# Performance work log

Measured on AMD Instinct MI355X. Metric: run time of the kernel, lower is better.

## Reference

```python
import jax, jax.numpy as jnp
import numpy as np

ALPHA = 0.2  # LeakyReLU negative slope
NEG_INF = -9e15


def setup_inputs() -> dict:
    key = jax.random.key(0)
    k1, k2, k3, k4, k5 = jax.random.split(key, 5)
    B, N, D = 4, 4096, 256
    feat = jax.random.normal(k1, (B, N, D), dtype=jnp.float32)
    adj = jax.random.randint(k2, (B, N, N), 0, 2, dtype=jnp.int32)
    W = jax.random.normal(k3, (D, D), dtype=jnp.float32) * (1.414 / np.sqrt(D))
    a_1 = jax.random.normal(k4, (D, 1), dtype=jnp.float32) * 0.1
    a_2 = jax.random.normal(k5, (D, 1), dtype=jnp.float32) * 0.1
    return {"feat": feat, "adj": adj, "W": W, "a_1": a_1, "a_2": a_2}


def reference(feat, adj, W, a_1, a_2):
    # h: [B, N, D]
    h = jnp.matmul(feat, W)
    Ax = jnp.matmul(h, a_1)  # [B, N, 1]
    Ay = jnp.matmul(h, a_2)  # [B, N, 1]
    # logits[b, i, j] = Ax[b, j] + Ay[b, i]
    logits = jnp.swapaxes(Ax, 1, 2) + Ay  # [B, N, N]
    e = jax.nn.leaky_relu(logits, negative_slope=ALPHA)
    e = jnp.where(adj > 0, e, jnp.float32(NEG_INF))
    attention = jax.nn.softmax(e, axis=-1)  # dropout p=0.0 -> identity
    h_prime = jnp.matmul(attention, feat)  # [B, N, in_features]
    h_out = jnp.matmul(h_prime, W)  # [B, N, out_features]
    return jax.nn.elu(h_out)
```

## Files before the change

kernel.cpp:

```cpp
#include <hip/hip_runtime.h>

typedef __attribute__((ext_vector_type(8))) short short8;
typedef __attribute__((ext_vector_type(4))) float f32x4;
typedef __attribute__((ext_vector_type(4))) int i32x4;
typedef __attribute__((ext_vector_type(2))) unsigned u32x2;

#define LOG2E 1.44269504f

__device__ __forceinline__ short f2bf(float f) {
  unsigned u = __builtin_bit_cast(unsigned, f);
  u += 0x7fffu + ((u >> 16) & 1u);
  return (short)(u >> 16);
}

__global__ void gat_wvec(const float* __restrict__ W, const float* __restrict__ a1,
                         const float* __restrict__ a2, float* __restrict__ w1,
                         float* __restrict__ w2) {
  __shared__ float a1f[256], a2f[256];
  const int tid = threadIdx.x;
  a1f[tid] = a1[tid];
  a2f[tid] = a2[tid];
  __syncthreads();
  float s1 = 0.f, s2 = 0.f;
  const float4* wr = (const float4*)(W + (size_t)tid * 256);
  for (int d0 = 0; d0 < 64; ++d0) {
    float4 v = wr[d0];
    s1 += v.x * a1f[d0 * 4] + v.y * a1f[d0 * 4 + 1] + v.z * a1f[d0 * 4 + 2] + v.w * a1f[d0 * 4 + 3];
    s2 += v.x * a2f[d0 * 4] + v.y * a2f[d0 * 4 + 1] + v.z * a2f[d0 * 4 + 2] + v.w * a2f[d0 * 4 + 3];
  }
  w1[tid] = s1;
  w2[tid] = s2;
}

__global__ void packB(const float* __restrict__ src, short* __restrict__ dst, int F) {
  const int tid = threadIdx.x;
  const int f = blockIdx.x, b = blockIdx.y;
  const int g = tid >> 4, l15 = tid & 15;
  const float* s = src + ((size_t)b * F * 32 + f * 32) * 256 + g * 16 + l15;
  short* d = dst + (((size_t)(b * F + f) * 16 + g) * 64) * 8;
#pragma unroll
  for (int q = 0; q < 4; ++q) {
    short8 v;
#pragma unroll
    for (int j8 = 0; j8 < 8; ++j8) v[j8] = f2bf(s[(q * 8 + j8) * 256]);
    *(short8*)(d + (q * 16 + l15) * 8) = v;
  }
}

__global__ void gat_axay(const float* __restrict__ feat, const float* __restrict__ w1,
                         const float* __restrict__ w2, float* __restrict__ AxL,
                         float* __restrict__ AyL) {
  const int lane = threadIdx.x & 63;
  const int row = blockIdx.x * 4 + (threadIdx.x >> 6);
  float4 fv = *(const float4*)(feat + (size_t)row * 256 + lane * 4);
  const float4 w1v = *(const float4*)(w1 + lane * 4);
  const float4 w2v = *(const float4*)(w2 + lane * 4);
  float s1 = fv.x * w1v.x + fv.y * w1v.y + fv.z * w1v.z + fv.w * w1v.w;
  float s2 = fv.x * w2v.x + fv.y * w2v.y + fv.z * w2v.z + fv.w * w2v.w;
#pragma unroll
  for (int off = 32; off >= 1; off >>= 1) {
    s1 += __shfl_xor(s1, off);
    s2 += __shfl_xor(s2, off);
  }
  if (lane == 0) { AxL[row] = s1 * LOG2E; AyL[row] = s2 * LOG2E; }
}

__global__ void gat_max(const float* __restrict__ AxL, float* __restrict__ MbL) {
  __shared__ float red[256];
  const int b = blockIdx.x, tid = threadIdx.x;
  float m = -3.4e38f;
  for (int i = tid; i < 4096; i += 256) m = fmaxf(m, AxL[b * 4096 + i]);
  red[tid] = m;
  __syncthreads();
  for (int s = 128; s > 0; s >>= 1) {
    if (tid < s) red[tid] = fmaxf(red[tid], red[tid + s]);
    __syncthreads();
  }
  if (tid == 0) MbL[b] = red[0];
}

__global__ __launch_bounds__(512, 4) void gat_attn(
    const short* __restrict__ featB,
    const int* __restrict__ adj,
    const float* __restrict__ AxL, const float* __restrict__ AyL,
    const float* __restrict__ MbL,
    const short* __restrict__ WB,
    float* __restrict__ out)
{
  __shared__ short smem[8448];

  const int tid = threadIdx.x;
  const int blk = blockIdx.x;
  const int x = blk & 7;
  const int b = x >> 1;
  const int it = ((blk >> 3) << 1) | (x & 1);
  const int i0 = it << 5;

  const int pi = tid >> 4;
  const int pj = tid & 15;
  const float ayL = AyL[b * 4096 + i0 + pi];
  const float sL = ayL + MbL[b];
  const float mrL = fmaxf(sL, 0.2f * sL);
  const float aL = ayL - mrL;
  const float dd = -0.8f * mrL;

  const int lane = tid & 63;
  const int w = tid >> 6;
  const int rowg = (w & 1) << 4;
  const int cgrp = (w >> 1) << 2;
  const int l15 = lane & 15;
  const int q = lane >> 4;

  f32x4 acc[4], lac;
  lac = (f32x4){0.f, 0.f, 0.f, 0.f};
#pragma unroll
  for (int j = 0; j < 4; ++j) acc[j] = (f32x4){0.f, 0.f, 0.f, 0.f};

  short8 ones;
#pragma unroll
  for (int j = 0; j < 8; ++j) ones[j] = (short)0x3F80;

  const i32x4* adjp = (const i32x4*)(adj + ((size_t)(b * 4096 + i0 + pi)) * 4096) + pj;
  const float4* axp = (const float4*)(AxL + b * 4096) + pj;
  const short* fbb = featB + (size_t)b * 128 * 16 * 64 * 8 + lane * 8;

  i32x4 adv = __builtin_nontemporal_load(adjp);
  float4 axv = axp[0];

  for (int jc = 0; jc < 64; ++jc) {
    const int pb = (jc & 1) * 2304;
    {
      const float* af = (const float*)&axv;
      unsigned pr[4];
#pragma unroll
      for (int u = 0; u < 4; ++u) {
        float v = af[u] + aL;
        float uu = fmaxf(v, fmaf(0.2f, v, dd));
        unsigned ub = adv[u] > 0 ? __builtin_bit_cast(unsigned, uu) : 0xFF800000u;
        float p = __builtin_amdgcn_exp2f(__builtin_bit_cast(float, ub));
        pr[u] = __builtin_bit_cast(unsigned, p) + 0x8000u;
      }
      u32x2 pw;
      pw[0] = __builtin_amdgcn_perm(pr[1], pr[0], 0x07060302u);
      pw[1] = __builtin_amdgcn_perm(pr[3], pr[2], 0x07060302u);
      *(u32x2*)(smem + pb + pi * 72 + pj * 4) = pw;
    }
    __syncthreads();

    if (jc < 63) {
      adv = __builtin_nontemporal_load(adjp + (jc + 1) * 16);
      axv = axp[(jc + 1) * 16];
    }

#pragma unroll
    for (int h = 0; h < 2; ++h) {
      const short* fb = fbb + (((size_t)(jc * 2 + h) * 16 + cgrp) << 9);
      short8 a = *(const short8*)(smem + pb + (rowg + l15) * 72 + h * 32 + q * 8);
      lac = __builtin_amdgcn_mfma_f32_16x16x32_bf16(a, ones, lac, 0, 0, 0);
#pragma unroll
      for (int ct = 0; ct < 4; ++ct) {
        short8 bf = *(const short8*)(fb + (ct << 9));
        acc[ct] = __builtin_amdgcn_mfma_f32_16x16x32_bf16(a, bf, acc[ct], 0, 0, 0);
      }
    }
  }

  float linv[4];
#pragma unroll
  for (int reg = 0; reg < 4; ++reg) {
    float l = lac[reg];
    linv[reg] = l > 0.f ? 1.f / l : 0.f;
  }

  __syncthreads();
  short* hbuf = smem;
#pragma unroll
  for (int reg = 0; reg < 4; ++reg) {
    const int lr = rowg + q * 4 + reg;
#pragma unroll
    for (int ct = 0; ct < 4; ++ct)
      hbuf[lr * 264 + cgrp * 16 + ct * 16 + l15] = f2bf(acc[ct][reg] * linv[reg]);
  }
  __syncthreads();

  f32x4 ac2[4];
#pragma unroll
  for (int j = 0; j < 4; ++j) ac2[j] = (f32x4){0.f, 0.f, 0.f, 0.f};

  const short* wbb = WB + lane * 8;
#pragma unroll
  for (int f = 0; f < 8; ++f) {
    short8 a = *(const short8*)&hbuf[(rowg + l15) * 264 + f * 32 + q * 8];
    const short* wb = wbb + (((size_t)f * 16 + cgrp) << 9);
#pragma unroll
    for (int ct = 0; ct < 4; ++ct) {
      short8 bf = *(const short8*)(wb + (ct << 9));
      ac2[ct] = __builtin_amdgcn_mfma_f32_16x16x32_bf16(a, bf, ac2[ct], 0, 0, 0);
    }
  }

#pragma unroll
  for (int reg = 0; reg < 4; ++reg) {
    const int row = i0 + rowg + q * 4 + reg;
    float* orow = out + ((size_t)(b * 4096 + row)) * 256 + cgrp * 16 + l15;
#pragma unroll
    for (int ct = 0; ct < 4; ++ct) {
      float v = ac2[ct][reg];
      float o = v > 0.f ? v : (__builtin_amdgcn_exp2f(v * LOG2E) - 1.f);
      __builtin_nontemporal_store(o, orow + ct * 16);
    }
  }
}

extern "C" void kernel_launch(void* const* d_in, const int* in_sizes, int n_in,
                              void* d_out, int out_size, void* d_ws, size_t ws_size,
                              hipStream_t stream) {
  (void)in_sizes; (void)n_in; (void)out_size; (void)ws_size;
  const float* feat = (const float*)d_in[0];
  const int* adj = (const int*)d_in[1];
  const float* W = (const float*)d_in[2];
  const float* a1 = (const float*)d_in[3];
  const float* a2 = (const float*)d_in[4];
  float* out = (float*)d_out;

  char* ws = (char*)d_ws;
  short* featB   = (short*)ws;
  short* WB      = (short*)(ws + 8388608);
  float* AxL     = (float*)(ws + 8519680);
  float* AyL     = (float*)(ws + 8585216);
  float* MbL     = (float*)(ws + 8650752);
  float* w1      = (float*)(ws + 8651776);
  float* w2      = (float*)(ws + 8652800);

  hipLaunchKernelGGL(gat_wvec, dim3(1), dim3(256), 0, stream, W, a1, a2, w1, w2);
  hipLaunchKernelGGL(packB, dim3(8, 1), dim3(256), 0, stream, W, WB, 8);
  hipLaunchKernelGGL(packB, dim3(128, 4), dim3(256), 0, stream, feat, featB, 128);
  hipLaunchKernelGGL(gat_axay, dim3(4096), dim3(256), 0, stream, feat, w1, w2, AxL, AyL);
  hipLaunchKernelGGL(gat_max, dim3(4), dim3(256), 0, stream, AxL, MbL);
  hipLaunchKernelGGL(gat_attn, dim3(512), dim3(512), 0, stream, featB, adj, AxL, AyL, MbL, WB, out);
}
```

Measured before the change: 476.7 us.

## Process 256-column adjacency chunks per step with staggered start per block

The attention loop now handles 256 columns per iteration (16 iterations) instead of 64 columns (64 iterations), with each wave loading four full adjacency rows of 1 KB each for coalesced access. The shared probability buffer is quadrupled and the start chunk is rotated per block so concurrent blocks read different featB slices. This is meant to cut the number of barriers and improve memory-level parallelism on the adj stream. In exchange it raises register pressure (four i32x4 prefetches) and LDS use, which may reduce occupancy under the 512x4 launch bounds.

```diff
diff --git a/kernel.cpp b/kernel.cpp
--- a/kernel.cpp
+++ b/kernel.cpp
@@ -87,7 +87,7 @@
     const short* __restrict__ WB,
     float* __restrict__ out)
 {
-  __shared__ short smem[8448];
+  __shared__ short smem[16896];
 
   const int tid = threadIdx.x;
   const int blk = blockIdx.x;
@@ -95,17 +95,24 @@
   const int b = x >> 1;
   const int it = ((blk >> 3) << 1) | (x & 1);
   const int i0 = it << 5;
-
-  const int pi = tid >> 4;
-  const int pj = tid & 15;
-  const float ayL = AyL[b * 4096 + i0 + pi];
-  const float sL = ayL + MbL[b];
-  const float mrL = fmaxf(sL, 0.2f * sL);
-  const float aL = ayL - mrL;
-  const float dd = -0.8f * mrL;
+  const int scoff = (blk >> 3) & 15;
 
   const int lane = tid & 63;
-  const int w = tid >> 6;
+  const int aw = tid >> 6;
+
+  float aLk[4], ddk[4];
+#pragma unroll
+  for (int k = 0; k < 4; ++k) {
+    float ayL = AyL[b * 4096 + i0 + aw * 4 + k];
+    float sL = ayL + MbL[b];
+    float mrL = fmaxf(sL, 0.2f * sL);
+    aLk[k] = ayL - mrL;
+    ddk[k] = -0.8f * mrL;
+  }
+  const int* adjr = adj + ((size_t)(b * 4096 + i0 + aw * 4)) * 4096 + lane * 4;
+  const float4* axp = (const float4*)(AxL + b * 4096) + lane;
+
+  const int w = aw;
   const int rowg = (w & 1) << 4;
   const int cgrp = (w >> 1) << 2;
   const int l15 = lane & 15;
@@ -120,42 +127,55 @@
 #pragma unroll
   for (int j = 0; j < 8; ++j) ones[j] = (short)0x3F80;
 
-  const i32x4* adjp = (const i32x4*)(adj + ((size_t)(b * 4096 + i0 + pi)) * 4096) + pj;
-  const float4* axp = (const float4*)(AxL + b * 4096) + pj;
   const short* fbb = featB + (size_t)b * 128 * 16 * 64 * 8 + lane * 8;
 
-  i32x4 adv = __builtin_nontemporal_load(adjp);
-  float4 axv = axp[0];
-
-  for (int jc = 0; jc < 64; ++jc) {
-    const int pb = (jc & 1) * 2304;
+  i32x4 adv[4];
+  float4 axv;
+  {
+    const int w0 = scoff;
+#pragma unroll
+    for (int k = 0; k < 4; ++k)
+      adv[k] = __builtin_nontemporal_load((const i32x4*)(adjr) + k * 1024 + w0 * 64);
+    axv = axp[w0 * 64];
+  }
+
+  for (int sc = 0; sc < 16; ++sc) {
+    const int wsc = (scoff + sc) & 15;
+    const int pb = (sc & 1) * 8448;
     {
       const float* af = (const float*)&axv;
-      unsigned pr[4];
-#pragma unroll
-      for (int u = 0; u < 4; ++u) {
-        float v = af[u] + aL;
-        float uu = fmaxf(v, fmaf(0.2f, v, dd));
-        unsigned ub = adv[u] > 0 ? __builtin_bit_cast(unsigned, uu) : 0xFF800000u;
-        float p = __builtin_amdgcn_exp2f(__builtin_bit_cast(float, ub));
-        pr[u] = __builtin_bit_cast(unsigned, p) + 0x8000u;
+#pragma unroll
+      for (int k = 0; k < 4; ++k) {
+        unsigned pr[4];
+#pragma unroll
+        for (int u = 0; u < 4; ++u) {
+          float v = af[u] + aLk[k];
+          float uu = fmaxf(v, fmaf(0.2f, v, ddk[k]));
+          unsigned ub = adv[k][u] > 0 ? __builtin_bit_cast(unsigned, uu) : 0xFF800000u;
+          float p = __builtin_amdgcn_exp2f(__builtin_bit_cast(float, ub));
+          pr[u] = __builtin_bit_cast(unsigned, p) + 0x8000u;
+        }
+        u32x2 pw;
+        pw[0] = __builtin_amdgcn_perm(pr[1], pr[0], 0x07060302u);
+        pw[1] = __builtin_amdgcn_perm(pr[3], pr[2], 0x07060302u);
+        *(u32x2*)(smem + pb + (aw * 4 + k) * 264 + lane * 4) = pw;
       }
-      u32x2 pw;
-      pw[0] = __builtin_amdgcn_perm(pr[1], pr[0], 0x07060302u);
-      pw[1] = __builtin_amdgcn_perm(pr[3], pr[2], 0x07060302u);
-      *(u32x2*)(smem + pb + pi * 72 + pj * 4) = pw;
     }
     __syncthreads();
 
-    if (jc < 63) {
-      adv = __builtin_nontemporal_load(adjp + (jc + 1) * 16);
-      axv = axp[(jc + 1) * 16];
-    }
-
-#pragma unroll
-    for (int h = 0; h < 2; ++h) {
-      const short* fb = fbb + (((size_t)(jc * 2 + h) * 16 + cgrp) << 9);
-      short8 a = *(const short8*)(smem + pb + (rowg + l15) * 72 + h * 32 + q * 8);
+    if (sc < 15) {
+      const int wn = (scoff + sc + 1) & 15;
+#pragma unroll
+      for (int k = 0; k < 4; ++k)
+        adv[k] = __builtin_nontemporal_load((const i32x4*)(adjr) + k * 1024 + wn * 64);
+      axv = axp[wn * 64];
+    }
+
+#pragma unroll
+    for (int h = 0; h < 8; ++h) {
+      const int f = wsc * 8 + h;
+      const short* fb = fbb + (((size_t)f * 16 + cgrp) << 9);
+      short8 a = *(const short8*)(smem + pb + (rowg + l15) * 264 + h * 32 + q * 8);
       lac = __builtin_amdgcn_mfma_f32_16x16x32_bf16(a, ones, lac, 0, 0, 0);
 #pragma unroll
       for (int ct = 0; ct < 4; ++ct) {
```

Result: faster. 446.1 us (-6.4%).
